# Optimization experiments

Hardware: AMD Instinct MI355X
Metric: run time of the kernel (lower is better)

Reference implementation:

```python
import jax, jax.numpy as jnp
import numpy as np

N_NODES = 50000
N_REL = 5
N_BASES = 5
OUT = 300
N_EDGES = 800000


def setup_inputs() -> dict:
    key = jax.random.key(0)
    ks = jax.random.split(key, 6)
    edge_index = jax.random.randint(ks[0], (2, N_EDGES), 0, N_NODES)
    edge_type = jax.random.randint(ks[1], (N_EDGES,), 0, N_REL)
    edge_norm = jax.random.normal(ks[2], (N_EDGES,), dtype=jnp.float32)
    # Learned params of RGCNConv(in=N_NODES, out=OUT, R=5, num_bases=5)
    basis = jax.random.normal(ks[3], (N_BASES, N_NODES, OUT), dtype=jnp.float32) * 0.02
    comp = jax.random.normal(ks[4], (N_REL, N_BASES), dtype=jnp.float32)
    root = jax.random.normal(ks[5], (N_NODES, OUT), dtype=jnp.float32) * 0.02
    bias = jnp.zeros((OUT,), dtype=jnp.float32)
    return dict(edge_index=edge_index, edge_type=edge_type, edge_norm=edge_norm,
                basis=basis, comp=comp, root=root, bias=bias)


def reference(edge_index, edge_type, edge_norm, basis, comp, root, bias):
    src, dst = edge_index[0], edge_index[1]
    # Basis decomposition: weight[r] = sum_b comp[r,b] * basis[b]  -> [R, N, OUT]
    weight = jnp.einsum('rb,bnd->rnd', comp, basis)
    # x=None => one-hot node features: per-edge message = weight[edge_type_e, src_e]
    msg = weight[edge_type, src]                                  # [E, OUT]
    # mean aggregation at destination (PyG RGCNConv default aggr='mean')
    agg = jax.ops.segment_sum(msg, dst, num_segments=N_NODES)     # [N, OUT]
    cnt = jax.ops.segment_sum(jnp.ones((msg.shape[0],), msg.dtype), dst,
                              num_segments=N_NODES)
    agg = agg / jnp.maximum(cnt, 1.0)[:, None]
    # root weight for one-hot x is a plain per-node row add, plus bias
    h = agg + root + bias
    return jax.nn.log_softmax(jax.nn.relu(h), axis=1)
```

## Files before the change

### kernel.cpp

```cpp
#include <hip/hip_runtime.h>
#include <hip/hip_bf16.h>
#include <hip/hip_fp16.h>
#include <string.h>

#define N_NODES 50000
#define N_REL 5
#define N_BASES 5
#define OUT 300
#define N_EDGES 800000
#define NBLK 196
#define BCAP 128

typedef float f4v __attribute__((ext_vector_type(4)));

__device__ __forceinline__ unsigned enc1(float x) {
    unsigned u = (unsigned)__half_as_ushort((__half)(x * 0.00390625f));
    unsigned s   = (u >> 15) & 1u;
    unsigned mag = u & 0x7fffu;
    unsigned m8  = (mag + 63u + ((mag >> 7) & 1u)) >> 7;
    return (s << 7) | m8;
}
__device__ __forceinline__ unsigned wenc(float x0, float x1, float x2, float x3) {
    return enc1(x0) | (enc1(x1) << 8) | (enc1(x2) << 16) | (enc1(x3) << 24);
}
__device__ __forceinline__ float2 dec2(unsigned v) {
    unsigned h = ((v & 0x80u)   << 8)  | ((v & 0x7fu)   << 7)
               | ((v & 0x8000u) << 16) | ((v & 0x7f00u) << 15);
    __half2 hh;
    memcpy(&hh, &h, 4);
    return __half22float2(hh);
}
__device__ __forceinline__ void wdec(unsigned w, float& x0, float& x1,
                                     float& x2, float& x3) {
    float2 lo = dec2(w);
    float2 hi = dec2(w >> 16);
    x0 = lo.x; x1 = lo.y; x2 = hi.x; x3 = hi.y;
}

__global__ void rgcn_zero(int* __restrict__ p, int n)
{
    int i = blockIdx.x * blockDim.x + threadIdx.x;
    if (i < n) p[i] = 0;
}

__global__ void rgcn_scatter_build(const float* __restrict__ basis,
                                   const float* __restrict__ comp,
                                   const int* __restrict__ srcA,
                                   const int* __restrict__ dstA,
                                   const int* __restrict__ typeA,
                                   int* __restrict__ cnt,
                                   int* __restrict__ bucket,
                                   unsigned* __restrict__ Wm,
                                   unsigned* __restrict__ Wt)
{
    const int gid = blockIdx.x * blockDim.x + threadIdx.x;
    const int gsz = gridDim.x * blockDim.x;

    for (int e = gid; e < N_EDGES; e += gsz) {
        const int d = dstA[e];
        const int pos = atomicAdd(&cnt[d], 1);
        if (pos < BCAP)
            bucket[d * BCAP + pos] = srcA[e] | (typeA[e] << 16);
    }

    float c[N_REL][N_BASES];
    #pragma unroll
    for (int t = 0; t < N_REL; ++t)
        #pragma unroll
        for (int b = 0; b < N_BASES; ++b)
            c[t][b] = comp[t * N_BASES + b];

    const int totm = N_NODES * 64;
    for (int id = gid; id < totm; id += gsz) {
        const int n = id >> 6;
        const int u = id & 63;
        const size_t eoff = (size_t)n * OUT + 4 * u;
        f4v f[N_BASES];
        #pragma unroll
        for (int b = 0; b < N_BASES; ++b)
            f[b] = __builtin_nontemporal_load(
                (const f4v*)&basis[(size_t)b * N_NODES * OUT + eoff]);
        #pragma unroll
        for (int t = 0; t < N_REL; ++t) {
            float x0 = 0.f, x1 = 0.f, x2 = 0.f, x3 = 0.f;
            #pragma unroll
            for (int b = 0; b < N_BASES; ++b) {
                x0 += c[t][b] * f[b].x; x1 += c[t][b] * f[b].y;
                x2 += c[t][b] * f[b].z; x3 += c[t][b] * f[b].w;
            }
            Wm[(size_t)t * N_NODES * 64 + id] = wenc(x0, x1, x2, x3);
        }
    }

    const int tott = N_NODES * 11;
    for (int id = gid; id < tott; id += gsz) {
        const int n = id / 11;
        const int v = id - n * 11;
        const size_t eoff = (size_t)n * OUT + 256 + 4 * v;
        f4v f[N_BASES];
        #pragma unroll
        for (int b = 0; b < N_BASES; ++b)
            f[b] = __builtin_nontemporal_load(
                (const f4v*)&basis[(size_t)b * N_NODES * OUT + eoff]);
        #pragma unroll
        for (int t = 0; t < N_REL; ++t) {
            float x0 = 0.f, x1 = 0.f, x2 = 0.f, x3 = 0.f;
            #pragma unroll
            for (int b = 0; b < N_BASES; ++b) {
                x0 += c[t][b] * f[b].x; x1 += c[t][b] * f[b].y;
                x2 += c[t][b] * f[b].z; x3 += c[t][b] * f[b].w;
            }
            Wt[(size_t)t * N_NODES * 11 + id] = wenc(x0, x1, x2, x3);
        }
    }
}

__global__ __launch_bounds__(256) void rgcn_aggregate(
    const int* __restrict__ cnt, const int* __restrict__ bucket,
    const unsigned* __restrict__ Wm, const unsigned* __restrict__ Wt,
    const float* __restrict__ root, const float* __restrict__ bias,
    float* __restrict__ out)
{
    __shared__ float smrow[4][304];
    const int lane = (int)(threadIdx.x & 63);
    const int wid  = (int)(threadIdx.x >> 6);
    const int k    = lane & 15;
    const int g    = lane >> 4;
    const int node = blockIdx.x * 4 + wid;
    const int deg = cnt[node];
    const int s = node * BCAP;
    const int e_end = s + min(deg, BCAP);
    const bool ktail = k < 11;

    float a[16];
    #pragma unroll
    for (int j = 0; j < 16; ++j) a[j] = 0.f;
    float t0 = 0.f, t1 = 0.f, t2 = 0.f, t3 = 0.f;

    const int nb4 = (min(deg, BCAP) + 3) >> 2;
    for (int bi = 0; bi < nb4; ++bi) {
        const int eidx = s + (bi << 2) + g;
        const bool act = eidx < e_end;
        const int p = bucket[act ? eidx : s];
        const unsigned r = (unsigned)(p >> 16) * N_NODES + (p & 0xFFFF);
        const uint4 w = *(const uint4*)&Wm[r * 64u + 4u * (unsigned)k];
        unsigned wt = 0u;
        if (ktail) wt = Wt[r * 11u + (unsigned)k];
        if (act) {
            float x0, x1, x2, x3;
            wdec(w.x, x0,x1,x2,x3); a[0]+=x0;  a[1]+=x1;  a[2]+=x2;  a[3]+=x3;
            wdec(w.y, x0,x1,x2,x3); a[4]+=x0;  a[5]+=x1;  a[6]+=x2;  a[7]+=x3;
            wdec(w.z, x0,x1,x2,x3); a[8]+=x0;  a[9]+=x1;  a[10]+=x2; a[11]+=x3;
            wdec(w.w, x0,x1,x2,x3); a[12]+=x0; a[13]+=x1; a[14]+=x2; a[15]+=x3;
            wdec(wt,  x0,x1,x2,x3); t0+=x0;    t1+=x1;    t2+=x2;    t3+=x3;
        }
    }

    #pragma unroll
    for (int j = 0; j < 16; ++j) {
        a[j] += __shfl_down(a[j], 32, 64);
        a[j] += __shfl_down(a[j], 16, 64);
    }
    t0 += __shfl_down(t0, 32, 64); t1 += __shfl_down(t1, 32, 64);
    t2 += __shfl_down(t2, 32, 64); t3 += __shfl_down(t3, 32, 64);
    t0 += __shfl_down(t0, 16, 64); t1 += __shfl_down(t1, 16, 64);
    t2 += __shfl_down(t2, 16, 64); t3 += __shfl_down(t3, 16, 64);

    if (lane < 16) {
        #pragma unroll
        for (int q = 0; q < 4; ++q) {
            float4 f4 = make_float4(a[4*q+0], a[4*q+1], a[4*q+2], a[4*q+3]);
            *(float4*)&smrow[wid][16 * lane + 4 * q] = f4;
        }
    }
    if (lane < 11)
        *(float4*)&smrow[wid][256 + 4 * lane] = make_float4(t0, t1, t2, t3);
    __builtin_amdgcn_wave_barrier();

    const float4 aa = *(const float4*)&smrow[wid][4 * lane];
    const bool tail = lane < 11;
    float4 tt = make_float4(0.f, 0.f, 0.f, 0.f);
    if (tail) tt = *(const float4*)&smrow[wid][256 + 4 * lane];

    const float inv = 256.0f / fmaxf((float)deg, 1.0f);
    const size_t ro = (size_t)node * OUT;
    const float4 rt0 = *(const float4*)&root[ro + 4 * lane];
    const float4 bi0 = *(const float4*)&bias[4 * lane];
    float v0 = fmaxf(aa.x * inv + rt0.x + bi0.x, 0.0f);
    float v1 = fmaxf(aa.y * inv + rt0.y + bi0.y, 0.0f);
    float v2 = fmaxf(aa.z * inv + rt0.z + bi0.z, 0.0f);
    float v3 = fmaxf(aa.w * inv + rt0.w + bi0.w, 0.0f);
    float v4 = 0.f, v5 = 0.f, v6 = 0.f, v7 = 0.f;
    if (tail) {
        const float4 rt1 = *(const float4*)&root[ro + 256 + 4 * lane];
        const float4 bi1 = *(const float4*)&bias[256 + 4 * lane];
        v4 = fmaxf(tt.x * inv + rt1.x + bi1.x, 0.0f);
        v5 = fmaxf(tt.y * inv + rt1.y + bi1.y, 0.0f);
        v6 = fmaxf(tt.z * inv + rt1.z + bi1.z, 0.0f);
        v7 = fmaxf(tt.w * inv + rt1.w + bi1.w, 0.0f);
    }
    float m = fmaxf(fmaxf(fmaxf(v0, v1), fmaxf(v2, v3)),
                    fmaxf(fmaxf(v4, v5), fmaxf(v6, v7)));
    #pragma unroll
    for (int off = 32; off >= 1; off >>= 1) m = fmaxf(m, __shfl_xor(m, off, 64));
    float sum = __expf(v0 - m) + __expf(v1 - m) + __expf(v2 - m) + __expf(v3 - m);
    if (tail) sum += __expf(v4 - m) + __expf(v5 - m) + __expf(v6 - m) + __expf(v7 - m);
    #pragma unroll
    for (int off = 32; off >= 1; off >>= 1) sum += __shfl_xor(sum, off, 64);
    const float lse = m + logf(sum);
    *(float4*)&out[ro + 4 * lane] =
        make_float4(v0 - lse, v1 - lse, v2 - lse, v3 - lse);
    if (tail)
        *(float4*)&out[ro + 256 + 4 * lane] =
            make_float4(v4 - lse, v5 - lse, v6 - lse, v7 - lse);
}

__global__ void rgcn_edge_scatter(const int* __restrict__ edge_index,
                                  const int* __restrict__ edge_type,
                                  const float* __restrict__ basis,
                                  const float* __restrict__ comp,
                                  float* __restrict__ agg,
                                  float* __restrict__ cnt)
{
    const int lane = threadIdx.x & 63;
    const int wid  = (blockIdx.x * (blockDim.x >> 6)) + (threadIdx.x >> 6);
    const int nwav = gridDim.x * (blockDim.x >> 6);
    const int* __restrict__ src_arr = edge_index;
    const int* __restrict__ dst_arr = edge_index + N_EDGES;
    for (int e = wid; e < N_EDGES; e += nwav) {
        const int src = src_arr[e];
        const int dst = dst_arr[e];
        const int t   = edge_type[e];
        const float c0 = comp[t*N_BASES+0], c1 = comp[t*N_BASES+1],
                    c2 = comp[t*N_BASES+2], c3 = comp[t*N_BASES+3],
                    c4 = comp[t*N_BASES+4];
        const size_t rowoff = (size_t)src * OUT;
        const float* b0 = basis + rowoff;
        const float* b1 = basis + (size_t)1*N_NODES*OUT + rowoff;
        const float* b2 = basis + (size_t)2*N_NODES*OUT + rowoff;
        const float* b3 = basis + (size_t)3*N_NODES*OUT + rowoff;
        const float* b4 = basis + (size_t)4*N_NODES*OUT + rowoff;
        float* aout = agg + (size_t)dst * OUT;
        for (int d = lane; d < OUT; d += 64) {
            float m = c0*b0[d] + c1*b1[d] + c2*b2[d] + c3*b3[d] + c4*b4[d];
            atomicAdd(&aout[d], m);
        }
        if (lane == 0) atomicAdd(&cnt[dst], 1.0f);
    }
}

__global__ void rgcn_finalize(float* __restrict__ agg,
                              const float* __restrict__ cnt,
                              const float* __restrict__ root,
                              const float* __restrict__ bias)
{
    const int lane = threadIdx.x & 63;
    const int wid  = (blockIdx.x * (blockDim.x >> 6)) + (threadIdx.x >> 6);
    if (wid >= N_NODES) return;
    const size_t rowoff = (size_t)wid * OUT;
    const float inv = 1.0f / fmaxf(cnt[wid], 1.0f);
    float v[5];
    float lmax = 0.0f;
    #pragma unroll
    for (int kk = 0; kk < 5; ++kk) {
        int d = lane + kk * 64;
        if (d < OUT) {
            float h = agg[rowoff + d] * inv + root[rowoff + d] + bias[d];
            float r = fmaxf(h, 0.0f);
            v[kk] = r; lmax = fmaxf(lmax, r);
        } else v[kk] = 0.0f;
    }
    #pragma unroll
    for (int off = 32; off >= 1; off >>= 1) lmax = fmaxf(lmax, __shfl_xor(lmax, off, 64));
    float lsum = 0.0f;
    #pragma unroll
    for (int kk = 0; kk < 5; ++kk) { int d = lane + kk*64; if (d < OUT) lsum += __expf(v[kk]-lmax); }
    #pragma unroll
    for (int off = 32; off >= 1; off >>= 1) lsum += __shfl_xor(lsum, off, 64);
    const float lse = lmax + logf(lsum);
    #pragma unroll
    for (int kk = 0; kk < 5; ++kk) { int d = lane + kk*64; if (d < OUT) agg[rowoff+d] = v[kk]-lse; }
}

extern "C" void kernel_launch(void* const* d_in, const int* in_sizes, int n_in,
                              void* d_out, int out_size, void* d_ws, size_t ws_size,
                              hipStream_t stream) {
    const int*   edge_index = (const int*)d_in[0];
    const int*   edge_type  = (const int*)d_in[1];
    const float* basis      = (const float*)d_in[3];
    const float* comp       = (const float*)d_in[4];
    const float* root       = (const float*)d_in[5];
    const float* bias       = (const float*)d_in[6];

    const size_t o_cnt    = 0;
    const size_t o_bucket = 200192;
    const size_t o_Wm     = 25800192;
    const size_t o_Wt     = 89800192;
    const size_t need     = o_Wt + (size_t)N_REL * N_NODES * 11 * sizeof(unsigned);

    if (ws_size >= need) {
        int*      cnt    = (int*)((char*)d_ws + o_cnt);
        int*      bucket = (int*)((char*)d_ws + o_bucket);
        unsigned* Wm     = (unsigned*)((char*)d_ws + o_Wm);
        unsigned* Wt     = (unsigned*)((char*)d_ws + o_Wt);

        rgcn_zero<<<NBLK, 256, 0, stream>>>(cnt, N_NODES);
        rgcn_scatter_build<<<12500, 256, 0, stream>>>(basis, comp,
                                                      edge_index,
                                                      edge_index + N_EDGES,
                                                      edge_type,
                                                      cnt, bucket, Wm, Wt);
        rgcn_aggregate<<<(N_NODES + 3) / 4, 256, 0, stream>>>(
            cnt, bucket, Wm, Wt, root, bias, (float*)d_out);
    } else {
        float* agg = (float*)d_out;
        float* cnt = (float*)d_ws;
        hipMemsetAsync(agg, 0, (size_t)out_size * sizeof(float), stream);
        hipMemsetAsync(cnt, 0, (size_t)N_NODES * sizeof(float), stream);
        rgcn_edge_scatter<<<4096, 256, 0, stream>>>(edge_index, edge_type, basis,
                                                    comp, agg, cnt);
        const int blocks = (N_NODES + 3) / 4;
        rgcn_finalize<<<blocks, 256, 0, stream>>>(agg, cnt, root, bias);
    }
}
```

Measured before the change: 186.4 us.

## Merge basis-combine loops, prefetch bucket indices via shuffle, hoist root loads

The build kernel folds its main and tail weight-combination loops into one grid-stride loop and raises the grid size so each thread does about one item. In the aggregate kernel, nodes with degree at most 64 load their whole bucket list once per wave and hand entries to lanes with shuffles, instead of issuing a dependent global load every iteration. The root and bias loads are moved before the edge loop so their latency overlaps the gather. This adds a branch inside the merged loop and a second code path in aggregation.

Result: slower. 190.7 us (+2.3%).

```diff
diff --git a/kernel.cpp b/kernel.cpp
--- a/kernel.cpp
+++ b/kernel.cpp
@@ -71,10 +71,16 @@
             c[t][b] = comp[t * N_BASES + b];
 
     const int totm = N_NODES * 64;
-    for (int id = gid; id < totm; id += gsz) {
-        const int n = id >> 6;
-        const int u = id & 63;
-        const size_t eoff = (size_t)n * OUT + 4 * u;
+    const int tota = totm + N_NODES * 11;
+    for (int id = gid; id < tota; id += gsz) {
+        size_t eoff;
+        if (id < totm) {
+            eoff = (size_t)(id >> 6) * OUT + 4 * (id & 63);
+        } else {
+            const int tid = id - totm;
+            const int n = tid / 11;
+            eoff = (size_t)n * OUT + 256 + 4 * (tid - n * 11);
+        }
         f4v f[N_BASES];
         #pragma unroll
         for (int b = 0; b < N_BASES; ++b)
@@ -88,29 +94,9 @@
                 x0 += c[t][b] * f[b].x; x1 += c[t][b] * f[b].y;
                 x2 += c[t][b] * f[b].z; x3 += c[t][b] * f[b].w;
             }
-            Wm[(size_t)t * N_NODES * 64 + id] = wenc(x0, x1, x2, x3);
-        }
-    }
-
-    const int tott = N_NODES * 11;
-    for (int id = gid; id < tott; id += gsz) {
-        const int n = id / 11;
-        const int v = id - n * 11;
-        const size_t eoff = (size_t)n * OUT + 256 + 4 * v;
-        f4v f[N_BASES];
-        #pragma unroll
-        for (int b = 0; b < N_BASES; ++b)
-            f[b] = __builtin_nontemporal_load(
-                (const f4v*)&basis[(size_t)b * N_NODES * OUT + eoff]);
-        #pragma unroll
-        for (int t = 0; t < N_REL; ++t) {
-            float x0 = 0.f, x1 = 0.f, x2 = 0.f, x3 = 0.f;
-            #pragma unroll
-            for (int b = 0; b < N_BASES; ++b) {
-                x0 += c[t][b] * f[b].x; x1 += c[t][b] * f[b].y;
-                x2 += c[t][b] * f[b].z; x3 += c[t][b] * f[b].w;
-            }
-            Wt[(size_t)t * N_NODES * 11 + id] = wenc(x0, x1, x2, x3);
+            const unsigned w = wenc(x0, x1, x2, x3);
+            if (id < totm) Wm[(size_t)t * N_NODES * 64 + id] = w;
+            else           Wt[(size_t)t * N_NODES * 11 + (id - totm)] = w;
         }
     }
 }
@@ -129,30 +115,63 @@
     const int node = blockIdx.x * 4 + wid;
     const int deg = cnt[node];
     const int s = node * BCAP;
-    const int e_end = s + min(deg, BCAP);
+    const int deg_c = min(deg, BCAP);
     const bool ktail = k < 11;
+    const bool tail = lane < 11;
+
+    const size_t ro = (size_t)node * OUT;
+    const float4 rt0 = *(const float4*)&root[ro + 4 * lane];
+    const float4 bi0 = *(const float4*)&bias[4 * lane];
+    float4 rt1 = make_float4(0.f,0.f,0.f,0.f), bi1 = rt1;
+    if (tail) {
+        rt1 = *(const float4*)&root[ro + 256 + 4 * lane];
+        bi1 = *(const float4*)&bias[256 + 4 * lane];
+    }
 
     float a[16];
     #pragma unroll
     for (int j = 0; j < 16; ++j) a[j] = 0.f;
     float t0 = 0.f, t1 = 0.f, t2 = 0.f, t3 = 0.f;
 
-    const int nb4 = (min(deg, BCAP) + 3) >> 2;
-    for (int bi = 0; bi < nb4; ++bi) {
-        const int eidx = s + (bi << 2) + g;
-        const bool act = eidx < e_end;
-        const int p = bucket[act ? eidx : s];
-        const unsigned r = (unsigned)(p >> 16) * N_NODES + (p & 0xFFFF);
-        const uint4 w = *(const uint4*)&Wm[r * 64u + 4u * (unsigned)k];
-        unsigned wt = 0u;
-        if (ktail) wt = Wt[r * 11u + (unsigned)k];
-        if (act) {
-            float x0, x1, x2, x3;
-            wdec(w.x, x0,x1,x2,x3); a[0]+=x0;  a[1]+=x1;  a[2]+=x2;  a[3]+=x3;
-            wdec(w.y, x0,x1,x2,x3); a[4]+=x0;  a[5]+=x1;  a[6]+=x2;  a[7]+=x3;
-            wdec(w.z, x0,x1,x2,x3); a[8]+=x0;  a[9]+=x1;  a[10]+=x2; a[11]+=x3;
-            wdec(w.w, x0,x1,x2,x3); a[12]+=x0; a[13]+=x1; a[14]+=x2; a[15]+=x3;
-            wdec(wt,  x0,x1,x2,x3); t0+=x0;    t1+=x1;    t2+=x2;    t3+=x3;
+    const int nb4 = (deg_c + 3) >> 2;
+    if (deg_c <= 64) {
+        const int clampL = (deg_c > 0) ? (deg_c - 1) : 0;
+        const int pre = bucket[s + min(lane, clampL)];
+        for (int bi = 0; bi < nb4; ++bi) {
+            const int idx4 = (bi << 2) + g;
+            const bool act = idx4 < deg_c;
+            const int p = __shfl(pre, min(idx4, clampL), 64);
+            const unsigned r = (unsigned)(p >> 16) * N_NODES + (p & 0xFFFF);
+            const uint4 w = *(const uint4*)&Wm[r * 64u + 4u * (unsigned)k];
+            unsigned wt = 0u;
+            if (ktail) wt = Wt[r * 11u + (unsigned)k];
+            if (act) {
+                float x0, x1, x2, x3;
+                wdec(w.x, x0,x1,x2,x3); a[0]+=x0;  a[1]+=x1;  a[2]+=x2;  a[3]+=x3;
+                wdec(w.y, x0,x1,x2,x3); a[4]+=x0;  a[5]+=x1;  a[6]+=x2;  a[7]+=x3;
+                wdec(w.z, x0,x1,x2,x3); a[8]+=x0;  a[9]+=x1;  a[10]+=x2; a[11]+=x3;
+                wdec(w.w, x0,x1,x2,x3); a[12]+=x0; a[13]+=x1; a[14]+=x2; a[15]+=x3;
+                wdec(wt,  x0,x1,x2,x3); t0+=x0;    t1+=x1;    t2+=x2;    t3+=x3;
+            }
+        }
+    } else {
+        const int e_end = s + deg_c;
+        for (int bi = 0; bi < nb4; ++bi) {
+            const int eidx = s + (bi << 2) + g;
+            const bool act = eidx < e_end;
+            const int p = bucket[act ? eidx : s];
+            const unsigned r = (unsigned)(p >> 16) * N_NODES + (p & 0xFFFF);
+            const uint4 w = *(const uint4*)&Wm[r * 64u + 4u * (unsigned)k];
+            unsigned wt = 0u;
+            if (ktail) wt = Wt[r * 11u + (unsigned)k];
+            if (act) {
+                float x0, x1, x2, x3;
+                wdec(w.x, x0,x1,x2,x3); a[0]+=x0;  a[1]+=x1;  a[2]+=x2;  a[3]+=x3;
+                wdec(w.y, x0,x1,x2,x3); a[4]+=x0;  a[5]+=x1;  a[6]+=x2;  a[7]+=x3;
+                wdec(w.z, x0,x1,x2,x3); a[8]+=x0;  a[9]+=x1;  a[10]+=x2; a[11]+=x3;
+                wdec(w.w, x0,x1,x2,x3); a[12]+=x0; a[13]+=x1; a[14]+=x2; a[15]+=x3;
+                wdec(wt,  x0,x1,x2,x3); t0+=x0;    t1+=x1;    t2+=x2;    t3+=x3;
+            }
         }
     }
 
@@ -178,22 +197,16 @@
     __builtin_amdgcn_wave_barrier();
 
     const float4 aa = *(const float4*)&smrow[wid][4 * lane];
-    const bool tail = lane < 11;
     float4 tt = make_float4(0.f, 0.f, 0.f, 0.f);
     if (tail) tt = *(const float4*)&smrow[wid][256 + 4 * lane];
 
     const float inv = 256.0f / fmaxf((float)deg, 1.0f);
-    const size_t ro = (size_t)node * OUT;
-    const float4 rt0 = *(const float4*)&root[ro + 4 * lane];
-    const float4 bi0 = *(const float4*)&bias[4 * lane];
     float v0 = fmaxf(aa.x * inv + rt0.x + bi0.x, 0.0f);
     float v1 = fmaxf(aa.y * inv + rt0.y + bi0.y, 0.0f);
     float v2 = fmaxf(aa.z * inv + rt0.z + bi0.z, 0.0f);
     float v3 = fmaxf(aa.w * inv + rt0.w + bi0.w, 0.0f);
     float v4 = 0.f, v5 = 0.f, v6 = 0.f, v7 = 0.f;
     if (tail) {
-        const float4 rt1 = *(const float4*)&root[ro + 256 + 4 * lane];
-        const float4 bi1 = *(const float4*)&bias[256 + 4 * lane];
         v4 = fmaxf(tt.x * inv + rt1.x + bi1.x, 0.0f);
         v5 = fmaxf(tt.y * inv + rt1.y + bi1.y, 0.0f);
         v6 = fmaxf(tt.z * inv + rt1.z + bi1.z, 0.0f);
@@ -305,7 +318,7 @@
         unsigned* Wt     = (unsigned*)((char*)d_ws + o_Wt);
 
         rgcn_zero<<<NBLK, 256, 0, stream>>>(cnt, N_NODES);
-        rgcn_scatter_build<<<12500, 256, 0, stream>>>(basis, comp,
+        rgcn_scatter_build<<<14649, 256, 0, stream>>>(basis, comp,
                                                       edge_index,
                                                       edge_index + N_EDGES,
                                                       edge_type,
```
